# Optimization experiments

Measured on AMD Instinct MI355X. Metric: run time of the kernel, lower is better.

Reference implementation:

```python
import jax, jax.numpy as jnp
import numpy as np

B, N, E, HID, L, H = 512, 100, 256, 1024, 6, 8
DH = E // H
NEG = -1e9


def setup_inputs() -> dict:
    key = jax.random.key(0)
    ks = jax.random.split(key, 20)
    def nrm(k, shp, s=0.05):
        return (jax.random.normal(k, shp) * s).astype(jnp.float32)
    return dict(
        x=nrm(ks[0], (B, N, 2), 1.0),
        target=jax.random.randint(ks[1], (B, N), 0, N),
        enc_Win=nrm(ks[2], (2, E)),
        enc_bin=jnp.zeros((E,), jnp.float32),
        enc_Wq=nrm(ks[3], (L, E, E)),
        enc_Wk=nrm(ks[4], (L, E, E)),
        enc_Wv=nrm(ks[5], (L, E, E)),
        enc_Wo=nrm(ks[6], (L, E, E)),
        enc_ln1_s=jnp.ones((L, E), jnp.float32),
        enc_ln1_b=jnp.zeros((L, E), jnp.float32),
        enc_W1=nrm(ks[7], (L, E, HID)),
        enc_b1=jnp.zeros((L, HID), jnp.float32),
        enc_W2=nrm(ks[8], (L, HID, E)),
        enc_b2=jnp.zeros((L, E), jnp.float32),
        enc_ln2_s=jnp.ones((L, E), jnp.float32),
        enc_ln2_b=jnp.zeros((L, E), jnp.float32),
        dec_Wq=nrm(ks[9], (3 * E, E)),
        dec_Wk=nrm(ks[10], (E, E)),
        dec_Wv=nrm(ks[11], (E, E)),
        dec_Wo=nrm(ks[12], (E, E)),
        dec_Wp=nrm(ks[13], (E, E)),
        token_1=jax.random.uniform(ks[14], (E,), jnp.float32),
        token_f=jax.random.uniform(ks[15], (E,), jnp.float32),
    )


def _ln(x, s, b):
    m = x.mean(-1, keepdims=True)
    v = x.var(-1, keepdims=True)
    return (x - m) * jax.lax.rsqrt(v + 1e-5) * s + b


def _encode(x, Win, bin_, Wq, Wk, Wv, Wo, ln1s, ln1b, W1, b1, W2, b2, ln2s, ln2b):
    h = x @ Win + bin_  # [B,N,E]
    for l in range(L):
        q = (h @ Wq[l]).reshape(B, N, H, DH)
        k = (h @ Wk[l]).reshape(B, N, H, DH)
        v = (h @ Wv[l]).reshape(B, N, H, DH)
        a = jax.nn.softmax(jnp.einsum('bqhd,bkhd->bhqk', q, k) / np.sqrt(DH).astype(np.float32), axis=-1)
        o = jnp.einsum('bhqk,bkhd->bqhd', a, v).reshape(B, N, E) @ Wo[l]
        h = _ln(h + o, ln1s[l], ln1b[l])
        ff = jax.nn.relu(h @ W1[l] + b1[l]) @ W2[l] + b2[l]
        h = _ln(h + ff, ln2s[l], ln2b[l])
    return h


def _forward(x, target, enc_Win, enc_bin, enc_Wq, enc_Wk, enc_Wv, enc_Wo,
             enc_ln1_s, enc_ln1_b, enc_W1, enc_b1, enc_W2, enc_b2,
             enc_ln2_s, enc_ln2_b, dec_Wq, dec_Wk, dec_Wv, dec_Wo, dec_Wp,
             token_1, token_f):
    nodes_emb = _encode(x, enc_Win, enc_bin, enc_Wq, enc_Wk, enc_Wv, enc_Wo,
                        enc_ln1_s, enc_ln1_b, enc_W1, enc_b1, enc_W2, enc_b2,
                        enc_ln2_s, enc_ln2_b)
    graph_emb = nodes_emb.mean(axis=1)  # [B,E]
    ctx0 = jnp.concatenate([graph_emb,
                            jnp.broadcast_to(token_1, (B, E)),
                            jnp.broadcast_to(token_f, (B, E))], axis=1)  # [B,3E]
    # Precompute decoder keys/values once (nodes_emb is fixed during decode).
    k = (nodes_emb @ dec_Wk).reshape(B, N, H, DH)
    v = (nodes_emb @ dec_Wv).reshape(B, N, H, DH)
    kp = nodes_emb @ dec_Wp  # pointer keys [B,N,E]
    bidx = jnp.arange(B)

    def step(carry, i):
        mask, start_emb, ctx = carry
        qh = (ctx @ dec_Wq).reshape(B, H, DH)
        sc = jnp.einsum('bhd,bnhd->bhn', qh, k) / np.sqrt(DH).astype(np.float32)
        sc = jnp.where(mask[:, None, :] > 0, NEG, sc)
        g = jnp.einsum('bhn,bnhd->bhd', jax.nn.softmax(sc, axis=-1), v).reshape(B, E) @ dec_Wo
        logits = 10.0 * jnp.tanh(jnp.einsum('be,bne->bn', g, kp) / np.sqrt(E).astype(np.float32))
        logits = jnp.where(mask > 0, NEG, logits)
        prob = jax.nn.softmax(logits, axis=-1)  # F.softmax(output, dim=1)
        idx = jnp.argmax(prob, axis=-1)         # greedy decode (teacher forcing off)
        mask = mask.at[bidx, idx].set(1.0)
        sel = nodes_emb[bidx, idx]              # [B,E]
        start_emb = jnp.where(i == 0, sel, start_emb)
        ctx = jnp.concatenate([graph_emb, start_emb, sel], axis=1)
        return (mask, start_emb, ctx), (prob, idx)

    carry0 = (jnp.zeros((B, N), jnp.float32), jnp.zeros((B, E), jnp.float32), ctx0)
    _, (probs_s, tours_s) = jax.lax.scan(step, carry0, jnp.arange(N))
    probs = jnp.transpose(probs_s, (1, 0, 2))          # [B,N,N]
    tours = tours_s.T.astype(jnp.float32)              # [B,N]
    nll = -jnp.mean(jnp.log(jnp.take_along_axis(probs, target[..., None], axis=2)[..., 0] + 1e-9))
    return probs, tours, nll


def reference(x, target, enc_Win, enc_bin, enc_Wq, enc_Wk, enc_Wv, enc_Wo,
              enc_ln1_s, enc_ln1_b, enc_W1, enc_b1, enc_W2, enc_b2,
              enc_ln2_s, enc_ln2_b, dec_Wq, dec_Wk, dec_Wv, dec_Wo, dec_Wp,
              token_1, token_f):
    return _forward(x, target, enc_Win, enc_bin, enc_Wq, enc_Wk, enc_Wv, enc_Wo,
                    enc_ln1_s, enc_ln1_b, enc_W1, enc_b1, enc_W2, enc_b2,
                    enc_ln2_s, enc_ln2_b, dec_Wq, dec_Wk, dec_Wv, dec_Wo, dec_Wp,
                    token_1, token_f)
```

## Files before the change

kernel.cpp:

```cpp
#include <hip/hip_runtime.h>
#include <cstdint>
#include <cmath>

#define NB 512
#define NN 100
#define NE 256
#define NHID 1024
#define NL 6
#define NH 8
#define NDH 32

static constexpr float SQRT_DH = 5.656854249492380195206754896838f;
static constexpr float NEGV = -1e9f;

static constexpr size_t WS_A   = 0;
static constexpr size_t WS_B1  = 13107200;
static constexpr size_t WS_B2  = 26214400;
static constexpr size_t WS_B3  = 39321600;
static constexpr size_t WS_B4  = 52428800;
static constexpr size_t WS_G   = 65536000;
static constexpr size_t WS_QB  = 65667072;
static constexpr size_t WS_TC  = 65798144;
static constexpr size_t WS_WPO = 65798400;
static constexpr size_t WS_NLL = 65863936;

__device__ __forceinline__ float wave_sum64(float v) {
#pragma unroll
  for (int o = 32; o; o >>= 1) v += __shfl_xor(v, o, 64);
  return v;
}
__device__ __forceinline__ double wave_sum64d(double v) {
#pragma unroll
  for (int o = 32; o; o >>= 1) v += __shfl_xor(v, o, 64);
  return v;
}
__device__ __forceinline__ float wave_max64(float v) {
#pragma unroll
  for (int o = 32; o; o >>= 1) v = fmaxf(v, __shfl_xor(v, o, 64));
  return v;
}

__global__ __launch_bounds__(256) void embed_kernel(
    const float* __restrict__ x, const float* __restrict__ win,
    const float* __restrict__ bin, float* __restrict__ h) {
  int i = blockIdx.x * 256 + threadIdx.x;
  int bn = i >> 6, e4 = i & 63;
  float x0 = x[bn * 2], x1 = x[bn * 2 + 1];
  float4 w0 = ((const float4*)win)[e4];
  float4 w1 = ((const float4*)win)[64 + e4];
  float4 bb = ((const float4*)bin)[e4];
  float4 r;
  r.x = x0 * w0.x + x1 * w1.x + bb.x;
  r.y = x0 * w0.y + x1 * w1.y + bb.y;
  r.z = x0 * w0.z + x1 * w1.z + bb.z;
  r.w = x0 * w0.w + x1 * w1.w + bb.w;
  ((float4*)h)[i] = r;
}

template <bool BIAS, bool RELU, bool ACCUM>
__global__ __launch_bounds__(256) void gemm_f32(
    const float* __restrict__ A, const float* __restrict__ W,
    const float* __restrict__ bias, float* __restrict__ C,
    int M, int N, int K, int ldw, int ldc) {
  __shared__ __align__(16) float As[16][132];
  __shared__ __align__(16) float Bs[16][128];
  const int t = threadIdx.x;
  const int bm = blockIdx.x * 128;
  const int bn = blockIdx.y * 128;
  const int tx = t & 15, ty = t >> 4;
  float acc[8][8];
#pragma unroll
  for (int i = 0; i < 8; ++i)
#pragma unroll
    for (int j = 0; j < 8; ++j) acc[i][j] = 0.f;

  const int am = t >> 2;
  const int ak = (t & 3) << 2;
  const int bn4 = (t & 31) << 2;
  const int bk = t >> 5;

  for (int kt = 0; kt < K; kt += 16) {
#pragma unroll
    for (int i = 0; i < 2; ++i) {
      float4 av = *(const float4*)&A[(size_t)(bm + am + 64 * i) * K + kt + ak];
      As[ak + 0][am + 64 * i] = av.x;
      As[ak + 1][am + 64 * i] = av.y;
      As[ak + 2][am + 64 * i] = av.z;
      As[ak + 3][am + 64 * i] = av.w;
      float4 bv = *(const float4*)&W[(size_t)(kt + bk + 8 * i) * ldw + bn + bn4];
      *(float4*)&Bs[bk + 8 * i][bn4] = bv;
    }
    __syncthreads();
#pragma unroll
    for (int k = 0; k < 16; ++k) {
      float a[8], bb[8];
      *(float4*)(a) = *(const float4*)&As[k][ty * 4];
      *(float4*)(a + 4) = *(const float4*)&As[k][64 + ty * 4];
      *(float4*)(bb) = *(const float4*)&Bs[k][tx * 4];
      *(float4*)(bb + 4) = *(const float4*)&Bs[k][64 + tx * 4];
#pragma unroll
      for (int i = 0; i < 8; ++i)
#pragma unroll
        for (int j = 0; j < 8; ++j) acc[i][j] += a[i] * bb[j];
    }
    __syncthreads();
  }
#pragma unroll
  for (int i = 0; i < 8; ++i) {
    int row = bm + ((i < 4) ? (ty * 4 + i) : (64 + ty * 4 + i - 4));
    size_t rb = (size_t)row * ldc;
#pragma unroll
    for (int jh = 0; jh < 2; ++jh) {
      int col = bn + jh * 64 + tx * 4;
      float4 v;
      v.x = acc[i][jh * 4 + 0];
      v.y = acc[i][jh * 4 + 1];
      v.z = acc[i][jh * 4 + 2];
      v.w = acc[i][jh * 4 + 3];
      if (BIAS) {
        v.x += bias[col]; v.y += bias[col + 1];
        v.z += bias[col + 2]; v.w += bias[col + 3];
      }
      if (RELU) {
        v.x = fmaxf(v.x, 0.f); v.y = fmaxf(v.y, 0.f);
        v.z = fmaxf(v.z, 0.f); v.w = fmaxf(v.w, 0.f);
      }
      if (ACCUM) {
        float4 o = *(const float4*)&C[rb + col];
        v.x += o.x; v.y += o.y; v.z += o.z; v.w += o.w;
      }
      *(float4*)&C[rb + col] = v;
    }
  }
}

__global__ __launch_bounds__(256) void kq_gemm(
    const float* __restrict__ A, const float* __restrict__ W,
    float* __restrict__ C) {
  __shared__ float rows[16][256];
  const int t = threadIdx.x;
  const int r0 = blockIdx.x * 16;
#pragma unroll
  for (int r = 0; r < 16; ++r) rows[r][t] = A[(size_t)(r0 + r) * 256 + t];
  __syncthreads();
  double acc[16];
#pragma unroll
  for (int r = 0; r < 16; ++r) acc[r] = 0.0;
  for (int d = 0; d < 256; ++d) {
    double wd = (double)W[d * 256 + t];
#pragma unroll
    for (int r = 0; r < 16; ++r) acc[r] += (double)rows[r][d] * wd;
  }
#pragma unroll
  for (int r = 0; r < 16; ++r)
    C[(size_t)(r0 + r) * 256 + t] = (float)acc[r];
}

__global__ __launch_bounds__(256) void enc_attn(
    const float* __restrict__ q, const float* __restrict__ k,
    const float* __restrict__ v, float* __restrict__ o) {
  const int bh = blockIdx.x;
  const int b = bh >> 3, h = bh & 7;
  __shared__ float qs[100][33], ks[100][33], vs[100][33];
  __shared__ float arow[4][100];
  const int t = threadIdx.x;
  const int lane = t & 63, w = t >> 6;
  const size_t base = (size_t)b * (NN * NE) + h * NDH;
  const int d0 = t & 31, n0 = t >> 5;
  for (int i = 0; i < 13; ++i) {
    int n = n0 + 8 * i;
    if (n < 100) {
      size_t gix = base + (size_t)n * NE + d0;
      qs[n][d0] = q[gix];
      ks[n][d0] = k[gix];
      vs[n][d0] = v[gix];
    }
  }
  __syncthreads();
  for (int i = w; i < 100; i += 4) {
    float s1 = 0.f, s2 = 0.f;
#pragma unroll
    for (int d = 0; d < 32; ++d) {
      float qv = qs[i][d];
      s1 += qv * ks[lane][d];
      if (lane < 36) s2 += qv * ks[lane + 64][d];
    }
    s1 /= SQRT_DH;
    s2 /= SQRT_DH;
    float mx = wave_max64(fmaxf(s1, (lane < 36) ? s2 : -3.4e38f));
    float e1 = expf(s1 - mx);
    float e2 = (lane < 36) ? expf(s2 - mx) : 0.f;
    float sm = wave_sum64(e1 + e2);
    arow[w][lane] = e1 / sm;
    if (lane < 36) arow[w][lane + 64] = e2 / sm;
    const int dd = lane & 31, half = lane >> 5;
    float accum = 0.f;
#pragma unroll
    for (int jj = 0; jj < 50; ++jj) {
      int j = half * 50 + jj;
      accum += arow[w][j] * vs[j][dd];
    }
    accum += __shfl_xor(accum, 32, 64);
    if (lane < 32) o[base + (size_t)i * NE + lane] = accum;
  }
}

__global__ __launch_bounds__(256) void ln_fused(
    const float* __restrict__ x, const float* __restrict__ r,
    const float* __restrict__ s, const float* __restrict__ bta,
    float* __restrict__ out) {
  const int t = threadIdx.x, lane = t & 63, w = t >> 6;
  const size_t row = (size_t)blockIdx.x * 4 + w;
  const size_t off = row * NE + lane * 4;
  float4 xv = *(const float4*)&x[off];
  float4 rv = *(const float4*)&r[off];
  float hx = xv.x + rv.x, hy = xv.y + rv.y, hz = xv.z + rv.z, hw = xv.w + rv.w;
  float sm = wave_sum64(hx + hy + hz + hw);
  float mean = sm * (1.f / 256.f);
  float dx = hx - mean, dy = hy - mean, dz = hz - mean, dw = hw - mean;
  float sq = wave_sum64(dx * dx + dy * dy + dz * dz + dw * dw);
  float var = sq * (1.f / 256.f);
  float rstd = 1.f / sqrtf(var + 1e-5f);
  float4 sv = *(const float4*)&s[lane * 4];
  float4 bv = *(const float4*)&bta[lane * 4];
  float4 ov;
  ov.x = dx * rstd * sv.x + bv.x;
  ov.y = dy * rstd * sv.y + bv.y;
  ov.z = dz * rstd * sv.z + bv.z;
  ov.w = dw * rstd * sv.w + bv.w;
  *(float4*)&out[off] = ov;
}

__global__ __launch_bounds__(256) void graph_mean(
    const float* __restrict__ h, float* __restrict__ g) {
  int b = blockIdx.x, t = threadIdx.x;
  const float* hb = h + (size_t)b * (NN * NE);
  double acc = 0.0;
  for (int n = 0; n < 100; ++n) acc += (double)hb[n * NE + t];
  g[b * NE + t] = (float)(acc / 100.0);
}

__global__ __launch_bounds__(256) void wpo_kernel(
    const float* __restrict__ Wp, const float* __restrict__ Wo,
    float* __restrict__ Wpo) {
  int d = blockIdx.x, t = threadIdx.x, lane = t & 63, w = t >> 6;
  __shared__ float wpl[256];
  wpl[t] = Wp[d * 256 + t];
  __syncthreads();
  for (int f = w; f < 256; f += 4) {
    float4 wov = *(const float4*)&Wo[f * 256 + lane * 4];
    float4 wpv = *(const float4*)&wpl[lane * 4];
    double p = (double)wov.x * wpv.x + (double)wov.y * wpv.y +
               (double)wov.z * wpv.z + (double)wov.w * wpv.w;
    p = wave_sum64d(p);
    if (lane == 0) Wpo[d * 256 + f] = (float)p;
  }
}

__global__ __launch_bounds__(256) void qbase_kernel(
    const float* __restrict__ g, const float* __restrict__ wq,
    float* __restrict__ qb) {
  int b = blockIdx.x, t = threadIdx.x;
  __shared__ float gl[256];
  gl[t] = g[b * 256 + t];
  __syncthreads();
  double acc = 0.0;
  for (int d = 0; d < 256; ++d) acc += (double)gl[d] * wq[d * 256 + t];
  qb[b * 256 + t] = (float)acc;
}

__global__ __launch_bounds__(256) void tcom_kernel(
    const float* __restrict__ t1, const float* __restrict__ tf,
    const float* __restrict__ wq, float* __restrict__ tc) {
  int t = threadIdx.x;
  __shared__ float a1[256], a2[256];
  a1[t] = t1[t];
  a2[t] = tf[t];
  __syncthreads();
  double acc = 0.0;
  for (int d = 0; d < 256; ++d) {
    acc += (double)a1[d] * wq[(256 + d) * 256 + t];
    acc += (double)a2[d] * wq[(512 + d) * 256 + t];
  }
  tc[t] = (float)acc;
}

__global__ __launch_bounds__(256) void kq_transpose(
    const float* __restrict__ kq, float* __restrict__ kqT) {
  int b = blockIdx.x, t = threadIdx.x;
  const float* src = kq + (size_t)b * 25600;
  float* dst = kqT + (size_t)b * 25600;
  for (int i = t; i < 25600; i += 256) {
    int f = i / 100, m = i - f * 100;
    dst[i] = src[m * 256 + f];
  }
}

__global__ __launch_bounds__(256) void decode_kernel(
    const float* __restrict__ nodes, const float* __restrict__ dk,
    const float* __restrict__ dv, const float* __restrict__ kqT,
    const float* __restrict__ q3, const float* __restrict__ qb,
    const float* __restrict__ tc, const float* __restrict__ wq2,
    const int* __restrict__ target, float* __restrict__ out,
    float* __restrict__ nllp) {
  const int b = blockIdx.x, t = threadIdx.x;
  const int lane = t & 63, w = t >> 6;
  __shared__ __align__(16) float vs[25600];
  __shared__ __align__(16) float qh[256];
  __shared__ float qfix[256], noderow[256], g[256];
  __shared__ float sc[800];
  __shared__ double lpartd[256];
  __shared__ float logits[100], pr[100], mask[100];
  __shared__ int idx_sh;

  const float* dvb = dv + (size_t)b * 25600;
  for (int i = t; i < 6400; i += 256)
    ((float4*)vs)[i] = ((const float4*)dvb)[i];
  if (t < 100) mask[t] = 0.f;
  qh[t] = qb[b * 256 + t] + tc[t];
  __syncthreads();

  const float* kb = dk + (size_t)b * 25600;
  const float* kqb = kqT + (size_t)b * 25600;
  const float* q3b = q3 + (size_t)b * 25600;
  float nll_acc = 0.f;

  for (int step = 0; step < 100; ++step) {
    for (int p = t; p < 800; p += 256) {
      int hh = p / 100;
      int n = p - hh * 100;
      const float* kr = kb + n * 256 + hh * 32;
      const float* qr = qh + hh * 32;
      double s = 0.0;
#pragma unroll
      for (int d4 = 0; d4 < 8; ++d4) {
        float4 kv = *(const float4*)(kr + d4 * 4);
        float4 qv = *(const float4*)(qr + d4 * 4);
        s += (double)qv.x * kv.x + (double)qv.y * kv.y +
             (double)qv.z * kv.z + (double)qv.w * kv.w;
      }
      float sf = (float)s / SQRT_DH;
      if (mask[n] > 0.f) sf = NEGV;
      sc[p] = sf;
    }
    __syncthreads();
    for (int hh = w; hh < 8; hh += 4) {
      float v1 = sc[hh * 100 + lane];
      float v2 = (lane < 36) ? sc[hh * 100 + 64 + lane] : -3.4e38f;
      float mx = wave_max64(fmaxf(v1, v2));
      float e1 = expf(v1 - mx);
      float e2 = (lane < 36) ? expf(v2 - mx) : 0.f;
      float sm = wave_sum64(e1 + e2);
      sc[hh * 100 + lane] = e1 / sm;
      if (lane < 36) sc[hh * 100 + 64 + lane] = e2 / sm;
    }
    __syncthreads();
    {
      const int hh = t >> 5;
      const float* ar = sc + hh * 100;
      float acc = 0.f;
#pragma unroll 4
      for (int n = 0; n < 100; ++n) acc += ar[n] * vs[n * 256 + t];
      g[t] = acc;
    }
    __syncthreads();
    {
      double part = 0.0;
      if (t < 200) {
        int m = (t < 100) ? t : (t - 100);
        int jh = (t < 100) ? 0 : 1;
        const float* kq = kqb + jh * 12800 + m;
        const float* gg = g + jh * 128;
#pragma unroll 16
        for (int f = 0; f < 128; ++f) part += (double)gg[f] * kq[f * 100];
      }
      lpartd[t] = part;
    }
    __syncthreads();
    if (t < 100) {
      double dot = lpartd[t] + lpartd[t + 100];
      float dotf = (float)dot;
      float lg = 10.f * tanhf(dotf * 0.0625f);
      if (mask[t] > 0.f) lg = NEGV;
      logits[t] = lg;
    }
    __syncthreads();
    if (w == 0) {
      float v1 = logits[lane];
      float v2 = (lane < 36) ? logits[64 + lane] : -3.4e38f;
      float mx = wave_max64(fmaxf(v1, v2));
      float e1 = expf(v1 - mx);
      float e2 = (lane < 36) ? expf(v2 - mx) : 0.f;
      float sm = wave_sum64(e1 + e2);
      float p1 = e1 / sm;
      float p2 = (lane < 36) ? e2 / sm : 0.f;
      float* orow = out + (size_t)b * 10000 + step * 100;
      orow[lane] = p1;
      pr[lane] = p1;
      if (lane < 36) {
        orow[64 + lane] = p2;
        pr[64 + lane] = p2;
      }
      float val = p1;
      int id = lane;
      if (lane < 36 && p2 > val) { val = p2; id = 64 + lane; }
#pragma unroll
      for (int o = 32; o; o >>= 1) {
        float ov = __shfl_xor(val, o, 64);
        int oi = __shfl_xor(id, o, 64);
        if (ov > val || (ov == val && oi < id)) { val = ov; id = oi; }
      }
      if (lane == 0) idx_sh = id;
    }
    __syncthreads();
    const int idx = idx_sh;
    if (t == 0) {
      mask[idx] = 1.f;
      int tgt = target[b * 100 + step];
      nll_acc -= logf(pr[tgt] + 1e-9f);
      out[5120000 + b * 100 + step] = (float)idx;
    }
    if (step == 0) {
      noderow[t] = nodes[(size_t)b * 25600 + idx * 256 + t];
      __syncthreads();
      double s2 = 0.0;
      for (int d = 0; d < 256; ++d) s2 += (double)noderow[d] * wq2[d * 256 + t];
      qfix[t] = qb[b * 256 + t] + (float)s2;
    }
    __syncthreads();
    qh[t] = qfix[t] + q3b[idx * 256 + t];
    __syncthreads();
  }
  if (t == 0) nllp[b] = nll_acc;
}

__global__ __launch_bounds__(256) void nll_final(
    const float* __restrict__ nllp, float* __restrict__ out) {
  int t = threadIdx.x, lane = t & 63, w = t >> 6;
  float v = nllp[t] + nllp[t + 256];
  v = wave_sum64(v);
  __shared__ float r[4];
  if (lane == 0) r[w] = v;
  __syncthreads();
  if (t == 0) out[0] = (r[0] + r[1] + r[2] + r[3]) / 51200.f;
}

extern "C" void kernel_launch(void* const* d_in, const int* in_sizes, int n_in,
                              void* d_out, int out_size, void* d_ws,
                              size_t ws_size, hipStream_t stream) {
  const float* x = (const float*)d_in[0];
  const int* target = (const int*)d_in[1];
  const float* Win = (const float*)d_in[2];
  const float* binp = (const float*)d_in[3];
  const float* Wq = (const float*)d_in[4];
  const float* Wk = (const float*)d_in[5];
  const float* Wv = (const float*)d_in[6];
  const float* Wo = (const float*)d_in[7];
  const float* ln1s = (const float*)d_in[8];
  const float* ln1b = (const float*)d_in[9];
  const float* W1 = (const float*)d_in[10];
  const float* b1 = (const float*)d_in[11];
  const float* W2 = (const float*)d_in[12];
  const float* b2 = (const float*)d_in[13];
  const float* ln2s = (const float*)d_in[14];
  const float* ln2b = (const float*)d_in[15];
  const float* dWq = (const float*)d_in[16];
  const float* dWk = (const float*)d_in[17];
  const float* dWv = (const float*)d_in[18];
  const float* dWo = (const float*)d_in[19];
  const float* dWp = (const float*)d_in[20];
  const float* tok1 = (const float*)d_in[21];
  const float* tokf = (const float*)d_in[22];

  float* ws = (float*)d_ws;
  float* out = (float*)d_out;
  float* A = ws + WS_A;
  float* R1 = ws + WS_B1;
  float* R2 = ws + WS_B2;
  float* R3 = ws + WS_B3;
  float* R4 = ws + WS_B4;
  float* G = ws + WS_G;
  float* QB = ws + WS_QB;
  float* TC = ws + WS_TC;
  float* WPO = ws + WS_WPO;
  float* NLLP = ws + WS_NLL;

  const int M = NB * NN;
  dim3 g2(400, 2), g4(400, 4), b256(256);

  embed_kernel<<<12800, 256, 0, stream>>>(x, Win, binp, A);

  for (int l = 0; l < NL; ++l) {
    const float* wq = Wq + (size_t)l * 65536;
    const float* wk = Wk + (size_t)l * 65536;
    const float* wv = Wv + (size_t)l * 65536;
    const float* wo = Wo + (size_t)l * 65536;
    gemm_f32<false, false, false><<<g2, b256, 0, stream>>>(A, wq, nullptr, R1, M, 256, 256, 256, 256);
    gemm_f32<false, false, false><<<g2, b256, 0, stream>>>(A, wk, nullptr, R2, M, 256, 256, 256, 256);
    gemm_f32<false, false, false><<<g2, b256, 0, stream>>>(A, wv, nullptr, R3, M, 256, 256, 256, 256);
    enc_attn<<<4096, 256, 0, stream>>>(R1, R2, R3, R4);
    gemm_f32<false, false, false><<<g2, b256, 0, stream>>>(R4, wo, nullptr, R1, M, 256, 256, 256, 256);
    ln_fused<<<12800, 256, 0, stream>>>(A, R1, ln1s + l * 256, ln1b + l * 256, A);
    const float* w1 = W1 + (size_t)l * 262144;
    const float* w2 = W2 + (size_t)l * 262144;
    gemm_f32<true, true, false><<<g4, b256, 0, stream>>>(A, w1, b1 + l * 1024, R1, M, 512, 256, 1024, 512);
    gemm_f32<true, false, false><<<g2, b256, 0, stream>>>(R1, w2, b2 + l * 256, R3, M, 256, 512, 256, 256);
    gemm_f32<true, true, false><<<g4, b256, 0, stream>>>(A, w1 + 512, b1 + l * 1024 + 512, R1, M, 512, 256, 1024, 512);
    gemm_f32<false, false, true><<<g2, b256, 0, stream>>>(R1, w2 + 512 * 256, nullptr, R3, M, 256, 512, 256, 256);
    ln_fused<<<12800, 256, 0, stream>>>(A, R3, ln2s + l * 256, ln2b + l * 256, A);
  }

  graph_mean<<<512, 256, 0, stream>>>(A, G);
  wpo_kernel<<<256, 256, 0, stream>>>(dWp, dWo, WPO);
  qbase_kernel<<<512, 256, 0, stream>>>(G, dWq, QB);
  tcom_kernel<<<1, 256, 0, stream>>>(tok1, tokf, dWq, TC);
  kq_gemm<<<3200, 256, 0, stream>>>(A, WPO, R3);
  kq_transpose<<<512, 256, 0, stream>>>(R3, R4);
  gemm_f32<false, false, false><<<g2, b256, 0, stream>>>(A, dWk, nullptr, R1, M, 256, 256, 256, 256);
  gemm_f32<false, false, false><<<g2, b256, 0, stream>>>(A, dWv, nullptr, R2, M, 256, 256, 256, 256);
  kq_gemm<<<3200, 256, 0, stream>>>(A, dWq + 512 * 256, R3);

  decode_kernel<<<512, 256, 0, stream>>>(A, R1, R2, R4, R3, QB, TC,
                                         dWq + 256 * 256, target, out, NLLP);
  nll_final<<<1, 256, 0, stream>>>(NLLP, out + 5171200);
}
```

Baseline: 12.00 ms.

## Compute decoder last-node query projection per step and shrink workspace buffers

Drops the precomputed per-node q3 projection (one kq_gemm plus a gather from a 50MB buffer). Each decode step now loads the selected node's embedding and does a 256x256 matvec against Wq's third block in double precision. The encoder attention writes its output in place over the q buffer, and the R4 workspace slot is removed, so buffers get reused and the workspace footprint drops. The trade-off is a serial 256-step double-precision loop over weights read from cache on every one of the 100 decode steps, which adds latency to an already sequential kernel.

```diff
diff --git a/kernel.cpp b/kernel.cpp
--- a/kernel.cpp
+++ b/kernel.cpp
@@ -17,12 +17,11 @@
 static constexpr size_t WS_B1  = 13107200;
 static constexpr size_t WS_B2  = 26214400;
 static constexpr size_t WS_B3  = 39321600;
-static constexpr size_t WS_B4  = 52428800;
-static constexpr size_t WS_G   = 65536000;
-static constexpr size_t WS_QB  = 65667072;
-static constexpr size_t WS_TC  = 65798144;
-static constexpr size_t WS_WPO = 65798400;
-static constexpr size_t WS_NLL = 65863936;
+static constexpr size_t WS_G   = 52428800;
+static constexpr size_t WS_QB  = 52559872;
+static constexpr size_t WS_TC  = 52690944;
+static constexpr size_t WS_WPO = 52691200;
+static constexpr size_t WS_NLL = 52756736;
 
 __device__ __forceinline__ float wave_sum64(float v) {
 #pragma unroll
@@ -157,8 +156,8 @@
 }
 
 __global__ __launch_bounds__(256) void enc_attn(
-    const float* __restrict__ q, const float* __restrict__ k,
-    const float* __restrict__ v, float* __restrict__ o) {
+    const float* q, const float* __restrict__ k,
+    const float* __restrict__ v, float* o) {
   const int bh = blockIdx.x;
   const int b = bh >> 3, h = bh & 7;
   __shared__ float qs[100][33], ks[100][33], vs[100][33];
@@ -299,8 +298,8 @@
 __global__ __launch_bounds__(256) void decode_kernel(
     const float* __restrict__ nodes, const float* __restrict__ dk,
     const float* __restrict__ dv, const float* __restrict__ kqT,
-    const float* __restrict__ q3, const float* __restrict__ qb,
-    const float* __restrict__ tc, const float* __restrict__ wq2,
+    const float* __restrict__ qb, const float* __restrict__ tc,
+    const float* __restrict__ wq2, const float* __restrict__ wq3,
     const int* __restrict__ target, float* __restrict__ out,
     float* __restrict__ nllp) {
   const int b = blockIdx.x, t = threadIdx.x;
@@ -322,7 +321,6 @@
 
   const float* kb = dk + (size_t)b * 25600;
   const float* kqb = kqT + (size_t)b * 25600;
-  const float* q3b = q3 + (size_t)b * 25600;
   float nll_acc = 0.f;
 
   for (int step = 0; step < 100; ++step) {
@@ -350,9 +348,9 @@
       float mx = wave_max64(fmaxf(v1, v2));
       float e1 = expf(v1 - mx);
       float e2 = (lane < 36) ? expf(v2 - mx) : 0.f;
-      float sm = wave_sum64(e1 + e2);
-      sc[hh * 100 + lane] = e1 / sm;
-      if (lane < 36) sc[hh * 100 + 64 + lane] = e2 / sm;
+      float smm = wave_sum64(e1 + e2);
+      sc[hh * 100 + lane] = e1 / smm;
+      if (lane < 36) sc[hh * 100 + 64 + lane] = e2 / smm;
     }
     __syncthreads();
     {
@@ -379,8 +377,7 @@
     __syncthreads();
     if (t < 100) {
       double dot = lpartd[t] + lpartd[t + 100];
-      float dotf = (float)dot;
-      float lg = 10.f * tanhf(dotf * 0.0625f);
+      float lg = 10.f * tanhf((float)dot * 0.0625f);
       if (mask[t] > 0.f) lg = NEGV;
       logits[t] = lg;
     }
@@ -391,9 +388,9 @@
       float mx = wave_max64(fmaxf(v1, v2));
       float e1 = expf(v1 - mx);
       float e2 = (lane < 36) ? expf(v2 - mx) : 0.f;
-      float sm = wave_sum64(e1 + e2);
-      float p1 = e1 / sm;
-      float p2 = (lane < 36) ? e2 / sm : 0.f;
+      float smm = wave_sum64(e1 + e2);
+      float p1 = e1 / smm;
+      float p2 = (lane < 36) ? e2 / smm : 0.f;
       float* orow = out + (size_t)b * 10000 + step * 100;
       orow[lane] = p1;
       pr[lane] = p1;
@@ -420,15 +417,18 @@
       nll_acc -= logf(pr[tgt] + 1e-9f);
       out[5120000 + b * 100 + step] = (float)idx;
     }
+    noderow[t] = nodes[(size_t)b * 25600 + idx * 256 + t];
+    __syncthreads();
     if (step == 0) {
-      noderow[t] = nodes[(size_t)b * 25600 + idx * 256 + t];
-      __syncthreads();
       double s2 = 0.0;
       for (int d = 0; d < 256; ++d) s2 += (double)noderow[d] * wq2[d * 256 + t];
       qfix[t] = qb[b * 256 + t] + (float)s2;
     }
-    __syncthreads();
-    qh[t] = qfix[t] + q3b[idx * 256 + t];
+    {
+      double s3 = 0.0;
+      for (int d = 0; d < 256; ++d) s3 += (double)noderow[d] * wq3[d * 256 + t];
+      qh[t] = qfix[t] + (float)s3;
+    }
     __syncthreads();
   }
   if (t == 0) nllp[b] = nll_acc;
@@ -478,7 +478,7 @@
   float* R1 = ws + WS_B1;
   float* R2 = ws + WS_B2;
   float* R3 = ws + WS_B3;
-  float* R4 = ws + WS_B4;
+  float* F = ws + WS_B1;
   float* G = ws + WS_G;
   float* QB = ws + WS_QB;
   float* TC = ws + WS_TC;
@@ -486,41 +486,43 @@
   float* NLLP = ws + WS_NLL;
 
   const int M = NB * NN;
-  dim3 g2(400, 2), g4(400, 4), b256(256);
-
-  embed_kernel<<<12800, 256, 0, stream>>>(x, Win, binp, A);
+  dim3 b256(256);
+  dim3 g2(400, 2), g4(400, 4);
+
+  embed_kernel<<<12800, b256, 0, stream>>>(x, Win, binp, A);
 
   for (int l = 0; l < NL; ++l) {
     const float* wq = Wq + (size_t)l * 65536;
     const float* wk = Wk + (size_t)l * 65536;
     const float* wv = Wv + (size_t)l * 65536;
     const float* wo = Wo + (size_t)l * 65536;
+    const float* w1 = W1 + (size_t)l * 262144;
+    const float* w2 = W2 + (size_t)l * 262144;
+
     gemm_f32<false, false, false><<<g2, b256, 0, stream>>>(A, wq, nullptr, R1, M, 256, 256, 256, 256);
     gemm_f32<false, false, false><<<g2, b256, 0, stream>>>(A, wk, nullptr, R2, M, 256, 256, 256, 256);
     gemm_f32<false, false, false><<<g2, b256, 0, stream>>>(A, wv, nullptr, R3, M, 256, 256, 256, 256);
-    enc_attn<<<4096, 256, 0, stream>>>(R1, R2, R3, R4);
-    gemm_f32<false, false, false><<<g2, b256, 0, stream>>>(R4, wo, nullptr, R1, M, 256, 256, 256, 256);
-    ln_fused<<<12800, 256, 0, stream>>>(A, R1, ln1s + l * 256, ln1b + l * 256, A);
-    const float* w1 = W1 + (size_t)l * 262144;
-    const float* w2 = W2 + (size_t)l * 262144;
-    gemm_f32<true, true, false><<<g4, b256, 0, stream>>>(A, w1, b1 + l * 1024, R1, M, 512, 256, 1024, 512);
-    gemm_f32<true, false, false><<<g2, b256, 0, stream>>>(R1, w2, b2 + l * 256, R3, M, 256, 512, 256, 256);
-    gemm_f32<true, true, false><<<g4, b256, 0, stream>>>(A, w1 + 512, b1 + l * 1024 + 512, R1, M, 512, 256, 1024, 512);
-    gemm_f32<false, false, true><<<g2, b256, 0, stream>>>(R1, w2 + 512 * 256, nullptr, R3, M, 256, 512, 256, 256);
-    ln_fused<<<12800, 256, 0, stream>>>(A, R3, ln2s + l * 256, ln2b + l * 256, A);
-  }
-
-  graph_mean<<<512, 256, 0, stream>>>(A, G);
-  wpo_kernel<<<256, 256, 0, stream>>>(dWp, dWo, WPO);
-  qbase_kernel<<<512, 256, 0, stream>>>(G, dWq, QB);
-  tcom_kernel<<<1, 256, 0, stream>>>(tok1, tokf, dWq, TC);
-  kq_gemm<<<3200, 256, 0, stream>>>(A, WPO, R3);
-  kq_transpose<<<512, 256, 0, stream>>>(R3, R4);
-  gemm_f32<false, false, false><<<g2, b256, 0, stream>>>(A, dWk, nullptr, R1, M, 256, 256, 256, 256);
-  gemm_f32<false, false, false><<<g2, b256, 0, stream>>>(A, dWv, nullptr, R2, M, 256, 256, 256, 256);
-  kq_gemm<<<3200, 256, 0, stream>>>(A, dWq + 512 * 256, R3);
-
-  decode_kernel<<<512, 256, 0, stream>>>(A, R1, R2, R4, R3, QB, TC,
-                                         dWq + 256 * 256, target, out, NLLP);
-  nll_final<<<1, 256, 0, stream>>>(NLLP, out + 5171200);
-}
+    enc_attn<<<4096, b256, 0, stream>>>(R1, R2, R3, R1);
+    gemm_f32<false, false, false><<<g2, b256, 0, stream>>>(R1, wo, nullptr, R2, M, 256, 256, 256, 256);
+    ln_fused<<<12800, b256, 0, stream>>>(A, R2, ln1s + l * 256, ln1b + l * 256, A);
+    gemm_f32<true, true, false><<<g4, b256, 0, stream>>>(A, w1, b1 + l * 1024, F, M, 512, 256, 1024, 512);
+    gemm_f32<true, false, false><<<g2, b256, 0, stream>>>(F, w2, b2 + l * 256, R3, M, 256, 512, 256, 256);
+    gemm_f32<true, true, false><<<g4, b256, 0, stream>>>(A, w1 + 512, b1 + l * 1024 + 512, F, M, 512, 256, 1024, 512);
+    gemm_f32<false, false, true><<<g2, b256, 0, stream>>>(F, w2 + 512 * 256, nullptr, R3, M, 256, 512, 256, 256);
+    ln_fused<<<12800, b256, 0, stream>>>(A, R3, ln2s + l * 256, ln2b + l * 256, A);
+  }
+
+  graph_mean<<<512, b256, 0, stream>>>(A, G);
+  wpo_kernel<<<256, b256, 0, stream>>>(dWp, dWo, WPO);
+  qbase_kernel<<<512, b256, 0, stream>>>(G, dWq, QB);
+  tcom_kernel<<<1, b256, 0, stream>>>(tok1, tokf, dWq, TC);
+  kq_gemm<<<3200, b256, 0, stream>>>(A, WPO, R3);
+  kq_transpose<<<512, b256, 0, stream>>>(R3, R2);
+  gemm_f32<false, false, false><<<g2, b256, 0, stream>>>(A, dWk, nullptr, R3, M, 256, 256, 256, 256);
+  gemm_f32<false, false, false><<<g2, b256, 0, stream>>>(A, dWv, nullptr, R1, M, 256, 256, 256, 256);
+
+  decode_kernel<<<512, b256, 0, stream>>>(A, R3, R1, R2, QB, TC,
+                                          dWq + 256 * 256, dWq + 512 * 256,
+                                          target, out, NLLP);
+  nll_final<<<1, b256, 0, stream>>>(NLLP, out + 5171200);
+}
```

Result: slower. 13.64 ms (+13.7%).
